# Kernel tuning notes

Hardware: AMD Instinct MI355X
Metric: run time of the kernel (lower is better)

## Reference

```python
import jax, jax.numpy as jnp
import numpy as np

B, T, D = 8, 4096, 1024
N_EXPERTS, N_SLOTS = 64, 8
HID = 256


def setup_inputs() -> dict:
    key = jax.random.key(0)
    ks = jax.random.split(key, 8)
    s = lambda *sh: 1.0 / np.sqrt(sh[-2]) if len(sh) >= 2 else 0.02
    tokens = jax.random.normal(ks[0], (B, T, D), dtype=jnp.float32)
    # routing weights, original uses np.random.random -> uniform [0,1); scale down for stability
    expert_mixture = jax.random.uniform(ks[1], (D, N_EXPERTS * N_SLOTS), dtype=jnp.float32) * 0.02
    W1 = jax.random.normal(ks[2], (N_EXPERTS, D, HID), dtype=jnp.float32) / np.sqrt(D)
    b1 = jnp.zeros((N_EXPERTS, HID), dtype=jnp.float32)
    W2 = jax.random.normal(ks[3], (N_EXPERTS, HID, HID), dtype=jnp.float32) / np.sqrt(HID)
    b2 = jnp.zeros((N_EXPERTS, HID), dtype=jnp.float32)
    W3 = jax.random.normal(ks[4], (N_EXPERTS, HID, D), dtype=jnp.float32) / np.sqrt(HID)
    b3 = jnp.zeros((N_EXPERTS, D), dtype=jnp.float32)
    return {"tokens": tokens, "expert_mixture": expert_mixture,
            "W1": W1, "b1": b1, "W2": W2, "b2": b2, "W3": W3, "b3": b3}


def reference(tokens, expert_mixture, W1, b1, W2, b2, W3, b3):
    b, t, d = tokens.shape
    flat = tokens.reshape(-1, d)                       # [BT, D]
    mat = flat @ expert_mixture                        # [BT, n*p]
    row_probs = jax.nn.softmax(mat, axis=0)            # over tokens
    col_probs = jax.nn.softmax(mat, axis=1)            # over slots
    x_hat = row_probs.T @ flat                         # [n*p, D] dispatch
    xs = x_hat.reshape(N_EXPERTS, N_SLOTS, d)          # [n, p, D]
    # per-expert MLP: Linear-ReLU-Linear-ReLU-Linear (batched over experts)
    h = jax.nn.relu(jnp.einsum('npd,ndh->nph', xs, W1) + b1[:, None, :])
    h = jax.nn.relu(jnp.einsum('nph,nhk->npk', h, W2) + b2[:, None, :])
    y_hat = jnp.einsum('npk,nkd->npd', h, W3) + b3[:, None, :]
    y_hat = y_hat.reshape(N_EXPERTS * N_SLOTS, d)      # [n*p, D]
    y = col_probs @ y_hat                              # [BT, D] combine
    return y.reshape(b, t, d)
```

## Files before the change

kernel.cpp:

```cpp
#include <hip/hip_runtime.h>
#include <math.h>

namespace {

constexpr int BT  = 8 * 4096;
constexpr int DIM = 1024;
constexpr int NE  = 64;
constexpr int NS  = 8;
constexpr int NP  = NE * NS;
constexpr int HID = 256;

typedef float f32x4 __attribute__((ext_vector_type(4)));
typedef __bf16 bf16x8 __attribute__((ext_vector_type(8)));
typedef short s16x8 __attribute__((ext_vector_type(8)));

__device__ __forceinline__ ushort f2bf(float x) {
  union { float f; unsigned u; } a; a.f = x;
  unsigned r = a.u + 0x7FFFu + ((a.u >> 16) & 1u);
  return (ushort)(r >> 16);
}
__device__ __forceinline__ float bf2f(ushort u) {
  union { unsigned u; float f; } a; a.u = (unsigned)u << 16;
  return a.f;
}

__device__ __forceinline__ void gload16(const void* g, void* l) {
  __builtin_amdgcn_global_load_lds(
      (const __attribute__((address_space(1))) void*)g,
      (__attribute__((address_space(3))) void*)l, 16, 0, 0);
}

template <bool ATOMIC, bool OBF, bool CSTAT>
__global__ __launch_bounds__(512) void k_gemm(const ushort* __restrict__ A,
                                              const ushort* __restrict__ Bt,
                                              void* __restrict__ Cv,
                                              int N, int kchunk,
                                              int lda, int ldb,
                                              float* __restrict__ pmOut,
                                              float* __restrict__ pzOut,
                                              float* __restrict__ rpmOut,
                                              float* __restrict__ rpzOut) {
  __shared__ __align__(16) ushort As0[256 * 64];
  __shared__ __align__(16) ushort As1[256 * 64];
  __shared__ __align__(16) ushort As2[256 * 64];
  __shared__ __align__(16) ushort Bs0[128 * 64];
  __shared__ __align__(16) ushort Bs1[128 * 64];
  __shared__ __align__(16) ushort Bs2[128 * 64];

  const int tid = threadIdx.x;
  const int wid = tid >> 6;
  const int lane = tid & 63;

  const int gx = gridDim.x, gy = gridDim.y;
  int wg = (blockIdx.z * gy + blockIdx.y) * gx + blockIdx.x;
  const int nwg = gx * gy * gridDim.z;
  wg = (wg & 7) * (nwg >> 3) + (wg >> 3);
  const int bx = wg % gx;
  const int rest = wg / gx;
  const int by = rest % gy;
  const int bz = rest / gy;

  const int n0 = bx * 128;
  const int m0 = by * 256;
  const int kb = bz * kchunk;

  const int w8 = wid * 8;
  const int lr = lane >> 3;
  const int ks = (((lane & 7) ^ lr) * 8);
  const ushort* Asrc = A + (size_t)(m0 + w8 + lr) * lda + ks;
  const ushort* Bsrc = Bt + (size_t)(n0 + w8 + lr) * ldb + ks;

  const int wm64 = (wid >> 1) * 64;
  const int wn64 = (wid & 1) * 64;
  const int fr = lane & 15;
  const int fq = lane >> 4;
  const int fq8 = fq * 8;
  const int frsw = (fr & 7) << 3;

  f32x4 acc[4][4];
#pragma unroll
  for (int i = 0; i < 4; ++i)
#pragma unroll
    for (int j = 0; j < 4; ++j) acc[i][j] = (f32x4){0.f, 0.f, 0.f, 0.f};

  const int nt = kchunk / 64;

#define STAGE6(An_, Bn_, kt_)                                                    \
  do {                                                                           \
    _Pragma("unroll") for (int q = 0; q < 4; ++q)                                \
      gload16(Asrc + (size_t)(q * 64) * lda + (kt_), (An_) + (q * 64 + w8) * 64);\
    _Pragma("unroll") for (int q = 0; q < 2; ++q)                                \
      gload16(Bsrc + (size_t)(q * 64) * ldb + (kt_), (Bn_) + (q * 64 + w8) * 64);\
  } while (0)

#define LD(B_, r_, h_)                                                          \
  __builtin_bit_cast(bf16x8, *(const s16x8*)((B_) + (size_t)(r_) * 64 +         \
                                             (((h_) * 32 + fq8) ^ frsw)))

#define GBLOCK(Ab_, Bb_, An_, Bn_, tt_)                                         \
  do {                                                                          \
    if ((tt_) + 1 < nt) asm volatile("s_waitcnt vmcnt(6)" ::: "memory");        \
    else                asm volatile("s_waitcnt vmcnt(0)" ::: "memory");        \
    __builtin_amdgcn_sched_barrier(0);                                          \
    __builtin_amdgcn_s_barrier();                                               \
    __builtin_amdgcn_sched_barrier(0);                                          \
    if ((tt_) + 2 < nt) STAGE6(An_, Bn_, kb + ((tt_) + 2) * 64);                \
    bf16x8 bfr_[4][2];                                                          \
    _Pragma("unroll") for (int n = 0; n < 4; ++n) {                             \
      bfr_[n][0] = LD(Bb_, wn64 + n * 16 + fr, 0);                              \
      bfr_[n][1] = LD(Bb_, wn64 + n * 16 + fr, 1);                              \
    }                                                                           \
    _Pragma("unroll") for (int m = 0; m < 4; ++m) {                             \
      bf16x8 a0_ = LD(Ab_, wm64 + m * 16 + fr, 0);                              \
      bf16x8 a1_ = LD(Ab_, wm64 + m * 16 + fr, 1);                              \
      __builtin_amdgcn_s_setprio(1);                                            \
      _Pragma("unroll") for (int n = 0; n < 4; ++n)                             \
        acc[m][n] = __builtin_amdgcn_mfma_f32_16x16x32_bf16(a0_, bfr_[n][0],    \
                                                            acc[m][n], 0, 0, 0);\
      _Pragma("unroll") for (int n = 0; n < 4; ++n)                             \
        acc[m][n] = __builtin_amdgcn_mfma_f32_16x16x32_bf16(a1_, bfr_[n][1],    \
                                                            acc[m][n], 0, 0, 0);\
      __builtin_amdgcn_s_setprio(0);                                            \
    }                                                                           \
  } while (0)

  STAGE6(As0, Bs0, kb);
  STAGE6(As1, Bs1, kb + 64);
  int t = 0;
  for (; t + 3 <= nt; t += 3) {
    GBLOCK(As0, Bs0, As2, Bs2, t);
    GBLOCK(As1, Bs1, As0, Bs0, t + 1);
    GBLOCK(As2, Bs2, As1, Bs1, t + 2);
  }
  if (t < nt) { GBLOCK(As0, Bs0, As2, Bs2, t); ++t; }
  if (t < nt) { GBLOCK(As1, Bs1, As0, Bs0, t); ++t; }
#undef GBLOCK
#undef LD
#undef STAGE6

  if (OBF) {
    ushort* Cb = (ushort*)Cv + (size_t)(m0 + wm64 + fq * 4) * N + n0 + wn64 + fr;
#pragma unroll
    for (int m = 0; m < 4; ++m)
#pragma unroll
      for (int n = 0; n < 4; ++n)
#pragma unroll
        for (int r = 0; r < 4; ++r)
          Cb[(size_t)(m * 16 + r) * N + n * 16] = f2bf(acc[m][n][r]);
  } else {
    float* Cb = (float*)Cv + (size_t)(m0 + wm64 + fq * 4) * N + n0 + wn64 + fr;
#pragma unroll
    for (int m = 0; m < 4; ++m)
#pragma unroll
      for (int n = 0; n < 4; ++n)
#pragma unroll
        for (int r = 0; r < 4; ++r) {
          float* p = Cb + (size_t)(m * 16 + r) * N + n * 16;
          if (ATOMIC) atomicAdd(p, acc[m][n][r]);
          else *p = acc[m][n][r];
        }
  }

  if (CSTAT) {
    float cm_[4], cz_[4];
#pragma unroll
    for (int n = 0; n < 4; ++n) { cm_[n] = -INFINITY; cz_[n] = 0.f; }
#pragma unroll
    for (int m = 0; m < 4; ++m)
#pragma unroll
      for (int n = 0; n < 4; ++n)
#pragma unroll
        for (int r = 0; r < 4; ++r) {
          float v = acc[m][n][r];
          float mm = fmaxf(cm_[n], v);
          cz_[n] = cz_[n] * __expf(cm_[n] - mm) + __expf(v - mm);
          cm_[n] = mm;
        }
#pragma unroll
    for (int off = 16; off <= 32; off <<= 1)
#pragma unroll
      for (int n = 0; n < 4; ++n) {
        float m2 = __shfl_xor(cm_[n], off);
        float z2 = __shfl_xor(cz_[n], off);
        float mm = fmaxf(cm_[n], m2);
        cz_[n] = cz_[n] * __expf(cm_[n] - mm) + z2 * __expf(m2 - mm);
        cm_[n] = mm;
      }
    float rm_[16], rz_[16];
#pragma unroll
    for (int m = 0; m < 4; ++m)
#pragma unroll
      for (int r = 0; r < 4; ++r) {
        const int i = m * 4 + r;
        float mx = fmaxf(fmaxf(acc[m][0][r], acc[m][1][r]),
                         fmaxf(acc[m][2][r], acc[m][3][r]));
        rm_[i] = mx;
        rz_[i] = __expf(acc[m][0][r] - mx) + __expf(acc[m][1][r] - mx) +
                 __expf(acc[m][2][r] - mx) + __expf(acc[m][3][r] - mx);
      }
#pragma unroll
    for (int off = 1; off <= 8; off <<= 1)
#pragma unroll
      for (int i = 0; i < 16; ++i) {
        float m2 = __shfl_xor(rm_[i], off);
        float z2 = __shfl_xor(rz_[i], off);
        float mm = fmaxf(rm_[i], m2);
        rz_[i] = rz_[i] * __expf(rm_[i] - mm) + z2 * __expf(m2 - mm);
        rm_[i] = mm;
      }
    __syncthreads();
    float* smx = (float*)As0;
    float* smz = smx + 4 * 128;
    float* smr = (float*)Bs0;
    float* smz2 = smr + 512;
    const int mrow = wid >> 1;
    if (lane < 16) {
#pragma unroll
      for (int n = 0; n < 4; ++n) {
        smx[mrow * 128 + wn64 + n * 16 + lane] = cm_[n];
        smz[mrow * 128 + wn64 + n * 16 + lane] = cz_[n];
      }
    }
    if (fr == 0) {
#pragma unroll
      for (int m = 0; m < 4; ++m)
#pragma unroll
        for (int r = 0; r < 4; ++r) {
          const int row = wm64 + m * 16 + fq * 4 + r;
          smr[(wid & 1) * 256 + row] = rm_[m * 4 + r];
          smz2[(wid & 1) * 256 + row] = rz_[m * 4 + r];
        }
    }
    __syncthreads();
    if (tid < 128) {
      float m = smx[tid], z = smz[tid];
#pragma unroll
      for (int p = 1; p < 4; ++p) {
        float m2 = smx[p * 128 + tid], z2 = smz[p * 128 + tid];
        float mm = fmaxf(m, m2);
        z = z * __expf(m - mm) + z2 * __expf(m2 - mm);
        m = mm;
      }
      pmOut[(size_t)by * NP + n0 + tid] = m;
      pzOut[(size_t)by * NP + n0 + tid] = z;
    }
    if (tid < 256) {
      float m1 = smr[tid], z1 = smz2[tid];
      float m2 = smr[256 + tid], z2 = smz2[256 + tid];
      float mm = fmaxf(m1, m2);
      float zz = z1 * __expf(m1 - mm) + z2 * __expf(m2 - mm);
      rpmOut[(size_t)bx * BT + m0 + tid] = mm;
      rpzOut[(size_t)bx * BT + m0 + tid] = zz;
    }
  }
}

__global__ __launch_bounds__(256) void k_convert(const float* __restrict__ X,
                                                 ushort* __restrict__ Y,
                                                 size_t n) {
  size_t i = ((size_t)blockIdx.x * 256 + threadIdx.x) * 8;
  const size_t stride = (size_t)gridDim.x * 256 * 8;
  for (; i < n; i += stride) {
    float4 a = *(const float4*)(X + i);
    float4 b = *(const float4*)(X + i + 4);
    s16x8 o;
    o[0] = (short)f2bf(a.x); o[1] = (short)f2bf(a.y);
    o[2] = (short)f2bf(a.z); o[3] = (short)f2bf(a.w);
    o[4] = (short)f2bf(b.x); o[5] = (short)f2bf(b.y);
    o[6] = (short)f2bf(b.z); o[7] = (short)f2bf(b.w);
    *(s16x8*)(Y + i) = o;
  }
}

__global__ __launch_bounds__(256) void k_tpose(const ushort* __restrict__ X,
                                               ushort* __restrict__ Yt,
                                               int Cc, int ldt) {
  __shared__ __align__(16) ushort tT[64][256];
  const int tid = threadIdx.x;
  const int r0 = blockIdx.x * 256, c0 = blockIdx.y * 64;
#pragma unroll
  for (int i = 0; i < 8; ++i) {
    const int idx = i * 256 + tid;
    const int r = idx >> 3, c8 = (idx & 7) * 8;
    s16x8 v = *(const s16x8*)(X + (size_t)(r0 + r) * Cc + c0 + c8);
#pragma unroll
    for (int j = 0; j < 8; ++j)
      tT[c8 + j][r ^ (((c8 + j) & 7) << 3)] = (ushort)v[j];
  }
  __syncthreads();
#pragma unroll
  for (int i = 0; i < 8; ++i) {
    const int idx = i * 256 + tid;
    const int c = idx >> 5, r8 = (idx & 31) * 8;
    s16x8 o = *(const s16x8*)&tT[c][r8 ^ ((c & 7) << 3)];
    *(s16x8*)(Yt + (size_t)(c0 + c) * ldt + r0 + r8) = o;
  }
}

template <bool ROWM, bool TRANSP>
__global__ __launch_bounds__(256) void k_cvt(const float* __restrict__ X,
                                             ushort* __restrict__ Yrm,
                                             ushort* __restrict__ Yt,
                                             int Cc, int ldt) {
  __shared__ __align__(16) ushort tT[64][256];
  const int tid = threadIdx.x;
  const int r0 = blockIdx.x * 256, c0 = blockIdx.y * 64;
#pragma unroll
  for (int i = 0; i < 16; ++i) {
    const int idx = i * 256 + tid;
    const int r = idx >> 4, c4 = (idx & 15) * 4;
    float4 v = *(const float4*)(X + (size_t)(r0 + r) * Cc + c0 + c4);
    ushort u[4] = {f2bf(v.x), f2bf(v.y), f2bf(v.z), f2bf(v.w)};
    if (ROWM) {
      ushort4 o = make_ushort4(u[0], u[1], u[2], u[3]);
      *(ushort4*)(Yrm + (size_t)(r0 + r) * Cc + c0 + c4) = o;
    }
    if (TRANSP) {
#pragma unroll
      for (int j = 0; j < 4; ++j)
        tT[c4 + j][r ^ (((c4 + j) & 7) << 3)] = u[j];
    }
  }
  if (TRANSP) {
    __syncthreads();
#pragma unroll
    for (int i = 0; i < 8; ++i) {
      const int idx = i * 256 + tid;
      const int c = idx >> 5, r8 = (idx & 31) * 8;
      s16x8 o = *(const s16x8*)&tT[c][r8 ^ ((c & 7) << 3)];
      *(s16x8*)(Yt + (size_t)(c0 + c) * ldt + r0 + r8) = o;
    }
  }
}

__global__ __launch_bounds__(256) void k_finals(const float* __restrict__ pm,
                                                const float* __restrict__ pz,
                                                const float* __restrict__ rpm,
                                                const float* __restrict__ rpz,
                                                float* __restrict__ colM,
                                                float* __restrict__ colIZ,
                                                float* __restrict__ rowM,
                                                float* __restrict__ rowIZ) {
  if (blockIdx.x < NP / 64) {
    const int col = blockIdx.x * 64 + (threadIdx.x & 63);
    const int q = threadIdx.x >> 6;
    float m = -INFINITY, z = 0.f;
    for (int r = q; r < BT / 256; r += 4) {
      float m2 = pm[(size_t)r * NP + col], z2 = pz[(size_t)r * NP + col];
      float mm = fmaxf(m, m2);
      z = z * __expf(m - mm) + z2 * __expf(m2 - mm);
      m = mm;
    }
    __shared__ float sm[4][64], sz[4][64];
    sm[q][threadIdx.x & 63] = m;
    sz[q][threadIdx.x & 63] = z;
    __syncthreads();
    if (q == 0) {
      for (int p = 1; p < 4; ++p) {
        float m2 = sm[p][threadIdx.x], z2 = sz[p][threadIdx.x];
        float mm = fmaxf(m, m2);
        z = z * __expf(m - mm) + z2 * __expf(m2 - mm);
        m = mm;
      }
      colM[col] = m;
      colIZ[col] = 1.f / z;
    }
  } else {
    const int t = (blockIdx.x - NP / 64) * 256 + threadIdx.x;
    float m = -INFINITY, z = 0.f;
#pragma unroll
    for (int c = 0; c < 4; ++c) {
      float m2 = rpm[(size_t)c * BT + t], z2 = rpz[(size_t)c * BT + t];
      float mm = fmaxf(m, m2);
      z = z * __expf(m - mm) + z2 * __expf(m2 - mm);
      m = mm;
    }
    rowM[t] = m;
    rowIZ[t] = 1.f / z;
  }
}

__global__ __launch_bounds__(256) void k_probs(const ushort* __restrict__ mat,
                                               const float* __restrict__ colM,
                                               const float* __restrict__ colIZ,
                                               const float* __restrict__ rowM,
                                               const float* __restrict__ rowIZ,
                                               ushort* __restrict__ Pc,
                                               ushort* __restrict__ Pt) {
  __shared__ __align__(16) ushort tT[64][256];
  __shared__ float cm[64], cz[64], rm[256], rz[256];
  const int tid = threadIdx.x;
  const int t0 = blockIdx.x * 256, s0 = blockIdx.y * 64;
  if (tid < 64) {
    cm[tid] = colM[s0 + tid];
    cz[tid] = colIZ[s0 + tid];
  }
  rm[tid] = rowM[t0 + tid];
  rz[tid] = rowIZ[t0 + tid];
  __syncthreads();
#pragma unroll
  for (int i = 0; i < 8; ++i) {
    const int idx = i * 256 + tid;
    const int r = idx >> 3, c8 = (idx & 7) * 8;
    s16x8 v = *(const s16x8*)(mat + (size_t)(t0 + r) * NP + s0 + c8);
    const float mr = rm[r], zr = rz[r];
    s16x8 oc;
#pragma unroll
    for (int j = 0; j < 8; ++j) {
      float f = bf2f((ushort)v[j]);
      oc[j] = (short)f2bf(__expf(f - mr) * zr);
      tT[c8 + j][r ^ (((c8 + j) & 7) << 3)] = f2bf(__expf(f - cm[c8 + j]) * cz[c8 + j]);
    }
    *(s16x8*)(Pc + (size_t)(t0 + r) * NP + s0 + c8) = oc;
  }
  __syncthreads();
#pragma unroll
  for (int i = 0; i < 8; ++i) {
    const int idx = i * 256 + tid;
    const int c = idx >> 5, r8 = (idx & 31) * 8;
    s16x8 o = *(const s16x8*)&tT[c][r8 ^ ((c & 7) << 3)];
    *(s16x8*)(Pt + (size_t)(s0 + c) * BT + t0 + r8) = o;
  }
}

__global__ __launch_bounds__(256) void k_binit3(const float* __restrict__ b1,
                                                const float* __restrict__ b2,
                                                const float* __restrict__ b3,
                                                float* __restrict__ base) {
  constexpr size_t XH = (size_t)NP * DIM;
  constexpr size_t H1 = (size_t)NP * HID;
  size_t idx = (size_t)blockIdx.x * 256 + threadIdx.x;
  if (idx < XH) { base[idx] = 0.f; return; }
  idx -= XH;
  if (idx < H1) { base[XH + idx] = b1[(idx / HID) / NS * HID + idx % HID]; return; }
  idx -= H1;
  if (idx < H1) { base[XH + H1 + idx] = b2[(idx / HID) / NS * HID + idx % HID]; return; }
  idx -= H1;
  base[XH + 2 * H1 + idx] = b3[(idx / DIM) / NS * DIM + idx % DIM];
}

template <int K, int N, int KS, bool RELU_IN>
__global__ __launch_bounds__(256) void k_mlp(const float* __restrict__ X,
                                             const float* __restrict__ W,
                                             float* __restrict__ Y) {
  constexpr int KSL = K / KS;
  __shared__ float xs[NS * KSL];
  const int tid = threadIdx.x;
  const int e = blockIdx.x;
  const int k0 = blockIdx.z * KSL;
  constexpr int T4 = (NS * KSL) / 4;
  for (int i = tid; i < T4; i += 256) {
    const int p = i / (KSL / 4), kk4 = (i % (KSL / 4)) * 4;
    float4 v = *(const float4*)(X + (size_t)(e * NS + p) * K + k0 + kk4);
    if (RELU_IN) {
      v.x = fmaxf(v.x, 0.f); v.y = fmaxf(v.y, 0.f);
      v.z = fmaxf(v.z, 0.f); v.w = fmaxf(v.w, 0.f);
    }
    *(float4*)(xs + p * KSL + kk4) = v;
  }
  __syncthreads();
  const int j = blockIdx.y * 64 + (tid & 63);
  const int pr = tid >> 6;
  const float* w = W + (size_t)e * K * N + (size_t)k0 * N + j;
  const float* x0 = xs + pr * KSL;
  const float* x1 = xs + (pr + 4) * KSL;
  float a0 = 0.f, a1 = 0.f;
#pragma unroll 8
  for (int k = 0; k < KSL; ++k) {
    float wv = w[(size_t)k * N];
    a0 += x0[k] * wv;
    a1 += x1[k] * wv;
  }
  atomicAdd(Y + (size_t)(e * NS + pr) * N + j, a0);
  atomicAdd(Y + (size_t)(e * NS + pr + 4) * N + j, a1);
}

}

extern "C" void kernel_launch(void* const* d_in, const int* in_sizes, int n_in,
                              void* d_out, int out_size, void* d_ws, size_t ws_size,
                              hipStream_t stream) {
  const float* tokens = (const float*)d_in[0];
  const float* em     = (const float*)d_in[1];
  const float* W1     = (const float*)d_in[2];
  const float* b1     = (const float*)d_in[3];
  const float* W2     = (const float*)d_in[4];
  const float* b2     = (const float*)d_in[5];
  const float* W3     = (const float*)d_in[6];
  const float* b3     = (const float*)d_in[7];
  float* out = (float*)d_out;

  char* w = (char*)d_ws;
  ushort* matb      = (ushort*)w; w += (size_t)BT * NP * 2;
  ushort* tokens_bf = (ushort*)w; w += (size_t)BT * DIM * 2;
  ushort* tokT      = (ushort*)w; w += (size_t)DIM * BT * 2;
  ushort* Pt        = (ushort*)w; w += (size_t)NP * BT * 2;
  ushort* Pc        = (ushort*)w; w += (size_t)BT * NP * 2;
  ushort* emT       = (ushort*)w; w += (size_t)NP * DIM * 2;
  ushort* yhatT     = (ushort*)w; w += (size_t)DIM * NP * 2;
  float*  pm        = (float*)w;  w += (size_t)(BT / 256) * NP * 4;
  float*  pz        = (float*)w;  w += (size_t)(BT / 256) * NP * 4;
  float*  rpm       = (float*)w;  w += (size_t)4 * BT * 4;
  float*  rpz       = (float*)w;  w += (size_t)4 * BT * 4;
  float*  colM      = (float*)w;  w += NP * 4;
  float*  colIZ     = (float*)w;  w += NP * 4;
  float*  rowM      = (float*)w;  w += BT * 4;
  float*  rowIZ     = (float*)w;  w += BT * 4;
  float*  xhat      = (float*)w;  w += (size_t)NP * DIM * 4;
  float*  h1        = (float*)w;  w += (size_t)NP * HID * 4;
  float*  h2        = (float*)w;  w += (size_t)NP * HID * 4;
  float*  yhat      = (float*)w;  w += (size_t)NP * DIM * 4;
  (void)ws_size; (void)in_sizes; (void)n_in; (void)out_size;

  k_convert<<<2048, 256, 0, stream>>>(tokens, tokens_bf, (size_t)BT * DIM);
  k_tpose<<<dim3(BT / 256, DIM / 64), 256, 0, stream>>>(tokens_bf, tokT, DIM, BT);
  k_cvt<false, true><<<dim3(DIM / 256, NP / 64), 256, 0, stream>>>(em, nullptr, emT, NP, DIM);
  k_gemm<false, true, true><<<dim3(NP / 128, BT / 256, 1), 512, 0, stream>>>(
      tokens_bf, emT, matb, NP, DIM, DIM, DIM, pm, pz, rpm, rpz);
  k_finals<<<NP / 64 + BT / 256, 256, 0, stream>>>(pm, pz, rpm, rpz, colM, colIZ, rowM, rowIZ);
  k_probs<<<dim3(BT / 256, NP / 64), 256, 0, stream>>>(matb, colM, colIZ, rowM, rowIZ, Pc, Pt);
  {
    constexpr size_t TOT = 2 * (size_t)NP * DIM + 2 * (size_t)NP * HID;
    k_binit3<<<(int)(TOT / 256), 256, 0, stream>>>(b1, b2, b3, xhat);
  }
  k_gemm<true, false, false><<<dim3(DIM / 128, NP / 256, 16), 512, 0, stream>>>(
      Pt, tokT, xhat, DIM, BT / 16, BT, BT, nullptr, nullptr, nullptr, nullptr);
  k_mlp<DIM, HID, 8, false><<<dim3(NE, HID / 64, 8), 256, 0, stream>>>(xhat, W1, h1);
  k_mlp<HID, HID, 4, true><<<dim3(NE, HID / 64, 4), 256, 0, stream>>>(h1, W2, h2);
  k_mlp<HID, DIM, 4, true><<<dim3(NE, DIM / 64, 4), 256, 0, stream>>>(h2, W3, yhat);
  k_cvt<false, true><<<dim3(NP / 256, DIM / 64), 256, 0, stream>>>(yhat, nullptr, yhatT, DIM, NP);
  k_gemm<false, false, false><<<dim3(DIM / 128, BT / 256, 1), 512, 0, stream>>>(
      Pc, yhatT, out, DIM, NP, NP, NP, nullptr, nullptr, nullptr, nullptr);
}
```

Before: 333.3 us.

## Fuse prep kernels and fold softmax finalization into split probability kernels

```diff
diff --git a/kernel.cpp b/kernel.cpp
--- a/kernel.cpp
+++ b/kernel.cpp
@@ -255,20 +255,74 @@
   }
 }
 
-__global__ __launch_bounds__(256) void k_convert(const float* __restrict__ X,
-                                                 ushort* __restrict__ Y,
-                                                 size_t n) {
-  size_t i = ((size_t)blockIdx.x * 256 + threadIdx.x) * 8;
-  const size_t stride = (size_t)gridDim.x * 256 * 8;
-  for (; i < n; i += stride) {
-    float4 a = *(const float4*)(X + i);
-    float4 b = *(const float4*)(X + i + 4);
-    s16x8 o;
-    o[0] = (short)f2bf(a.x); o[1] = (short)f2bf(a.y);
-    o[2] = (short)f2bf(a.z); o[3] = (short)f2bf(a.w);
-    o[4] = (short)f2bf(b.x); o[5] = (short)f2bf(b.y);
-    o[6] = (short)f2bf(b.z); o[7] = (short)f2bf(b.w);
-    *(s16x8*)(Y + i) = o;
+__global__ __launch_bounds__(256) void k_prep(const float* __restrict__ tokens,
+                                              const float* __restrict__ em,
+                                              const float* __restrict__ b1,
+                                              const float* __restrict__ b2,
+                                              const float* __restrict__ b3,
+                                              ushort* __restrict__ tokens_bf,
+                                              ushort* __restrict__ emT,
+                                              float* __restrict__ base) {
+  __shared__ __align__(16) ushort tT[64][256];
+  const int tid = threadIdx.x;
+  const int bid = blockIdx.x;
+  if (bid < 2048) {
+    const size_t n = (size_t)BT * DIM;
+    size_t i = ((size_t)bid * 256 + tid) * 8;
+    const size_t stride = (size_t)2048 * 256 * 8;
+    for (; i < n; i += stride) {
+      float4 a = *(const float4*)(tokens + i);
+      float4 b = *(const float4*)(tokens + i + 4);
+      s16x8 o;
+      o[0] = (short)f2bf(a.x); o[1] = (short)f2bf(a.y);
+      o[2] = (short)f2bf(a.z); o[3] = (short)f2bf(a.w);
+      o[4] = (short)f2bf(b.x); o[5] = (short)f2bf(b.y);
+      o[6] = (short)f2bf(b.z); o[7] = (short)f2bf(b.w);
+      *(s16x8*)(tokens_bf + i) = o;
+    }
+  } else if (bid < 2080) {
+    const int b = bid - 2048;
+    const int r0 = (b >> 3) * 256, c0 = (b & 7) * 64;
+#pragma unroll
+    for (int i = 0; i < 16; ++i) {
+      const int idx = i * 256 + tid;
+      const int r = idx >> 4, c4 = (idx & 15) * 4;
+      float4 v = *(const float4*)(em + (size_t)(r0 + r) * NP + c0 + c4);
+      ushort u[4] = {f2bf(v.x), f2bf(v.y), f2bf(v.z), f2bf(v.w)};
+#pragma unroll
+      for (int j = 0; j < 4; ++j)
+        tT[c4 + j][r ^ (((c4 + j) & 7) << 3)] = u[j];
+    }
+    __syncthreads();
+#pragma unroll
+    for (int i = 0; i < 8; ++i) {
+      const int idx = i * 256 + tid;
+      const int c = idx >> 5, r8 = (idx & 31) * 8;
+      s16x8 o = *(const s16x8*)&tT[c][r8 ^ ((c & 7) << 3)];
+      *(s16x8*)(emT + (size_t)(c0 + c) * DIM + r0 + r8) = o;
+    }
+  } else {
+    constexpr size_t XH = (size_t)NP * DIM;
+    constexpr size_t H1 = (size_t)NP * HID;
+    constexpr size_t TOT4 = (2 * XH + 2 * H1) / 4;
+    size_t i = (size_t)(bid - 2080) * 256 + tid;
+    for (; i < TOT4; i += (size_t)1024 * 256) {
+      const size_t idx = i * 4;
+      float4 v;
+      if (idx < XH) {
+        v = make_float4(0.f, 0.f, 0.f, 0.f);
+      } else if (idx < XH + H1) {
+        const size_t k = idx - XH;
+        v = *(const float4*)(b1 + (k / HID) / NS * HID + k % HID);
+      } else if (idx < XH + 2 * H1) {
+        const size_t k = idx - XH - H1;
+        v = *(const float4*)(b2 + (k / HID) / NS * HID + k % HID);
+      } else {
+        const size_t k = idx - XH - 2 * H1;
+        v = *(const float4*)(b3 + (k / DIM) / NS * DIM + k % DIM);
+      }
+      *(float4*)(base + idx) = v;
+    }
   }
 }
 
@@ -297,11 +351,9 @@
   }
 }
 
-template <bool ROWM, bool TRANSP>
-__global__ __launch_bounds__(256) void k_cvt(const float* __restrict__ X,
-                                             ushort* __restrict__ Yrm,
-                                             ushort* __restrict__ Yt,
-                                             int Cc, int ldt) {
+__global__ __launch_bounds__(256) void k_cvtT(const float* __restrict__ X,
+                                              ushort* __restrict__ Yt,
+                                              int Cc, int ldt) {
   __shared__ __align__(16) ushort tT[64][256];
   const int tid = threadIdx.x;
   const int r0 = blockIdx.x * 256, c0 = blockIdx.y * 64;
@@ -311,39 +363,67 @@
     const int r = idx >> 4, c4 = (idx & 15) * 4;
     float4 v = *(const float4*)(X + (size_t)(r0 + r) * Cc + c0 + c4);
     ushort u[4] = {f2bf(v.x), f2bf(v.y), f2bf(v.z), f2bf(v.w)};
-    if (ROWM) {
-      ushort4 o = make_ushort4(u[0], u[1], u[2], u[3]);
-      *(ushort4*)(Yrm + (size_t)(r0 + r) * Cc + c0 + c4) = o;
-    }
-    if (TRANSP) {
-#pragma unroll
-      for (int j = 0; j < 4; ++j)
-        tT[c4 + j][r ^ (((c4 + j) & 7) << 3)] = u[j];
-    }
-  }
-  if (TRANSP) {
-    __syncthreads();
-#pragma unroll
-    for (int i = 0; i < 8; ++i) {
-      const int idx = i * 256 + tid;
-      const int c = idx >> 5, r8 = (idx & 31) * 8;
-      s16x8 o = *(const s16x8*)&tT[c][r8 ^ ((c & 7) << 3)];
-      *(s16x8*)(Yt + (size_t)(c0 + c) * ldt + r0 + r8) = o;
-    }
-  }
-}
-
-__global__ __launch_bounds__(256) void k_finals(const float* __restrict__ pm,
-                                                const float* __restrict__ pz,
-                                                const float* __restrict__ rpm,
-                                                const float* __restrict__ rpz,
-                                                float* __restrict__ colM,
-                                                float* __restrict__ colIZ,
-                                                float* __restrict__ rowM,
-                                                float* __restrict__ rowIZ) {
-  if (blockIdx.x < NP / 64) {
-    const int col = blockIdx.x * 64 + (threadIdx.x & 63);
-    const int q = threadIdx.x >> 6;
+#pragma unroll
+    for (int j = 0; j < 4; ++j)
+      tT[c4 + j][r ^ (((c4 + j) & 7) << 3)] = u[j];
+  }
+  __syncthreads();
+#pragma unroll
+  for (int i = 0; i < 8; ++i) {
+    const int idx = i * 256 + tid;
+    const int c = idx >> 5, r8 = (idx & 31) * 8;
+    s16x8 o = *(const s16x8*)&tT[c][r8 ^ ((c & 7) << 3)];
+    *(s16x8*)(Yt + (size_t)(c0 + c) * ldt + r0 + r8) = o;
+  }
+}
+
+__global__ __launch_bounds__(256) void k_probs_c(const ushort* __restrict__ mat,
+                                                 const float* __restrict__ rpm,
+                                                 const float* __restrict__ rpz,
+                                                 ushort* __restrict__ Pc) {
+  __shared__ float rm[64], rz[64];
+  const int tid = threadIdx.x;
+  const int t0 = blockIdx.x * 64;
+  if (tid < 64) {
+    const int t = t0 + tid;
+    float m = -INFINITY, z = 0.f;
+#pragma unroll
+    for (int c = 0; c < 4; ++c) {
+      float m2 = rpm[(size_t)c * BT + t], z2 = rpz[(size_t)c * BT + t];
+      float mm = fmaxf(m, m2);
+      z = z * __expf(m - mm) + z2 * __expf(m2 - mm);
+      m = mm;
+    }
+    rm[tid] = m;
+    rz[tid] = 1.f / z;
+  }
+  __syncthreads();
+#pragma unroll
+  for (int i = 0; i < 16; ++i) {
+    const int idx = i * 256 + tid;
+    const int r = idx >> 6, c8 = (idx & 63) * 8;
+    s16x8 v = *(const s16x8*)(mat + (size_t)(t0 + r) * NP + c8);
+    const float mr = rm[r], zr = rz[r];
+    s16x8 oc;
+#pragma unroll
+    for (int j = 0; j < 8; ++j)
+      oc[j] = (short)f2bf(__expf(bf2f((ushort)v[j]) - mr) * zr);
+    *(s16x8*)(Pc + (size_t)(t0 + r) * NP + c8) = oc;
+  }
+}
+
+__global__ __launch_bounds__(256) void k_probs_t(const ushort* __restrict__ mat,
+                                                 const float* __restrict__ pm,
+                                                 const float* __restrict__ pz,
+                                                 ushort* __restrict__ Pt) {
+  __shared__ __align__(16) ushort tT[64][256];
+  __shared__ float cm[64], cz[64];
+  __shared__ float sm[4][64], sz[4][64];
+  const int tid = threadIdx.x;
+  const int t0 = blockIdx.x * 256, s0 = blockIdx.y * 64;
+  {
+    const int col = s0 + (tid & 63);
+    const int q = tid >> 6;
     float m = -INFINITY, z = 0.f;
     for (int r = q; r < BT / 256; r += 4) {
       float m2 = pm[(size_t)r * NP + col], z2 = pz[(size_t)r * NP + col];
@@ -351,67 +431,32 @@
       z = z * __expf(m - mm) + z2 * __expf(m2 - mm);
       m = mm;
     }
-    __shared__ float sm[4][64], sz[4][64];
-    sm[q][threadIdx.x & 63] = m;
-    sz[q][threadIdx.x & 63] = z;
-    __syncthreads();
-    if (q == 0) {
-      for (int p = 1; p < 4; ++p) {
-        float m2 = sm[p][threadIdx.x], z2 = sz[p][threadIdx.x];
-        float mm = fmaxf(m, m2);
-        z = z * __expf(m - mm) + z2 * __expf(m2 - mm);
-        m = mm;
-      }
-      colM[col] = m;
-      colIZ[col] = 1.f / z;
-    }
-  } else {
-    const int t = (blockIdx.x - NP / 64) * 256 + threadIdx.x;
-    float m = -INFINITY, z = 0.f;
-#pragma unroll
-    for (int c = 0; c < 4; ++c) {
-      float m2 = rpm[(size_t)c * BT + t], z2 = rpz[(size_t)c * BT + t];
+    sm[q][tid & 63] = m;
+    sz[q][tid & 63] = z;
+  }
+  __syncthreads();
+  if (tid < 64) {
+    float m = sm[0][tid], z = sz[0][tid];
+#pragma unroll
+    for (int p = 1; p < 4; ++p) {
+      float m2 = sm[p][tid], z2 = sz[p][tid];
       float mm = fmaxf(m, m2);
       z = z * __expf(m - mm) + z2 * __expf(m2 - mm);
       m = mm;
     }
-    rowM[t] = m;
-    rowIZ[t] = 1.f / z;
-  }
-}
-
-__global__ __launch_bounds__(256) void k_probs(const ushort* __restrict__ mat,
-                                               const float* __restrict__ colM,
-                                               const float* __restrict__ colIZ,
-                                               const float* __restrict__ rowM,
-                                               const float* __restrict__ rowIZ,
-                                               ushort* __restrict__ Pc,
-                                               ushort* __restrict__ Pt) {
-  __shared__ __align__(16) ushort tT[64][256];
-  __shared__ float cm[64], cz[64], rm[256], rz[256];
-  const int tid = threadIdx.x;
-  const int t0 = blockIdx.x * 256, s0 = blockIdx.y * 64;
-  if (tid < 64) {
-    cm[tid] = colM[s0 + tid];
-    cz[tid] = colIZ[s0 + tid];
-  }
-  rm[tid] = rowM[t0 + tid];
-  rz[tid] = rowIZ[t0 + tid];
+    cm[tid] = m;
+    cz[tid] = 1.f / z;
+  }
   __syncthreads();
 #pragma unroll
   for (int i = 0; i < 8; ++i) {
     const int idx = i * 256 + tid;
     const int r = idx >> 3, c8 = (idx & 7) * 8;
     s16x8 v = *(const s16x8*)(mat + (size_t)(t0 + r) * NP + s0 + c8);
-    const float mr = rm[r], zr = rz[r];
-    s16x8 oc;
-#pragma unroll
-    for (int j = 0; j < 8; ++j) {
-      float f = bf2f((ushort)v[j]);
-      oc[j] = (short)f2bf(__expf(f - mr) * zr);
-      tT[c8 + j][r ^ (((c8 + j) & 7) << 3)] = f2bf(__expf(f - cm[c8 + j]) * cz[c8 + j]);
-    }
-    *(s16x8*)(Pc + (size_t)(t0 + r) * NP + s0 + c8) = oc;
+#pragma unroll
+    for (int j = 0; j < 8; ++j)
+      tT[c8 + j][r ^ (((c8 + j) & 7) << 3)] =
+          f2bf(__expf(bf2f((ushort)v[j]) - cm[c8 + j]) * cz[c8 + j]);
   }
   __syncthreads();
 #pragma unroll
@@ -421,22 +466,6 @@
     s16x8 o = *(const s16x8*)&tT[c][r8 ^ ((c & 7) << 3)];
     *(s16x8*)(Pt + (size_t)(s0 + c) * BT + t0 + r8) = o;
   }
-}
-
-__global__ __launch_bounds__(256) void k_binit3(const float* __restrict__ b1,
-                                                const float* __restrict__ b2,
-                                                const float* __restrict__ b3,
-                                                float* __restrict__ base) {
-  constexpr size_t XH = (size_t)NP * DIM;
-  constexpr size_t H1 = (size_t)NP * HID;
-  size_t idx = (size_t)blockIdx.x * 256 + threadIdx.x;
-  if (idx < XH) { base[idx] = 0.f; return; }
-  idx -= XH;
-  if (idx < H1) { base[XH + idx] = b1[(idx / HID) / NS * HID + idx % HID]; return; }
-  idx -= H1;
-  if (idx < H1) { base[XH + H1 + idx] = b2[(idx / HID) / NS * HID + idx % HID]; return; }
-  idx -= H1;
-  base[XH + 2 * H1 + idx] = b3[(idx / DIM) / NS * DIM + idx % DIM];
 }
 
 template <int K, int N, int KS, bool RELU_IN>
@@ -502,33 +531,24 @@
   float*  pz        = (float*)w;  w += (size_t)(BT / 256) * NP * 4;
   float*  rpm       = (float*)w;  w += (size_t)4 * BT * 4;
   float*  rpz       = (float*)w;  w += (size_t)4 * BT * 4;
-  float*  colM      = (float*)w;  w += NP * 4;
-  float*  colIZ     = (float*)w;  w += NP * 4;
-  float*  rowM      = (float*)w;  w += BT * 4;
-  float*  rowIZ     = (float*)w;  w += BT * 4;
   float*  xhat      = (float*)w;  w += (size_t)NP * DIM * 4;
   float*  h1        = (float*)w;  w += (size_t)NP * HID * 4;
   float*  h2        = (float*)w;  w += (size_t)NP * HID * 4;
   float*  yhat      = (float*)w;  w += (size_t)NP * DIM * 4;
   (void)ws_size; (void)in_sizes; (void)n_in; (void)out_size;
 
-  k_convert<<<2048, 256, 0, stream>>>(tokens, tokens_bf, (size_t)BT * DIM);
+  k_prep<<<3104, 256, 0, stream>>>(tokens, em, b1, b2, b3, tokens_bf, emT, xhat);
   k_tpose<<<dim3(BT / 256, DIM / 64), 256, 0, stream>>>(tokens_bf, tokT, DIM, BT);
-  k_cvt<false, true><<<dim3(DIM / 256, NP / 64), 256, 0, stream>>>(em, nullptr, emT, NP, DIM);
   k_gemm<false, true, true><<<dim3(NP / 128, BT / 256, 1), 512, 0, stream>>>(
       tokens_bf, emT, matb, NP, DIM, DIM, DIM, pm, pz, rpm, rpz);
-  k_finals<<<NP / 64 + BT / 256, 256, 0, stream>>>(pm, pz, rpm, rpz, colM, colIZ, rowM, rowIZ);
-  k_probs<<<dim3(BT / 256, NP / 64), 256, 0, stream>>>(matb, colM, colIZ, rowM, rowIZ, Pc, Pt);
-  {
-    constexpr size_t TOT = 2 * (size_t)NP * DIM + 2 * (size_t)NP * HID;
-    k_binit3<<<(int)(TOT / 256), 256, 0, stream>>>(b1, b2, b3, xhat);
-  }
+  k_probs_c<<<BT / 64, 256, 0, stream>>>(matb, rpm, rpz, Pc);
+  k_probs_t<<<dim3(BT / 256, NP / 64), 256, 0, stream>>>(matb, pm, pz, Pt);
   k_gemm<true, false, false><<<dim3(DIM / 128, NP / 256, 16), 512, 0, stream>>>(
       Pt, tokT, xhat, DIM, BT / 16, BT, BT, nullptr, nullptr, nullptr, nullptr);
   k_mlp<DIM, HID, 8, false><<<dim3(NE, HID / 64, 8), 256, 0, stream>>>(xhat, W1, h1);
   k_mlp<HID, HID, 4, true><<<dim3(NE, HID / 64, 4), 256, 0, stream>>>(h1, W2, h2);
   k_mlp<HID, DIM, 4, true><<<dim3(NE, DIM / 64, 4), 256, 0, stream>>>(h2, W3, yhat);
-  k_cvt<false, true><<<dim3(NP / 256, DIM / 64), 256, 0, stream>>>(yhat, nullptr, yhatT, DIM, NP);
+  k_cvtT<<<dim3(NP / 256, DIM / 64), 256, 0, stream>>>(yhat, yhatT, DIM, NP);
   k_gemm<false, false, false><<<dim3(DIM / 128, BT / 256, 1), 512, 0, stream>>>(
       Pc, yhatT, out, DIM, NP, NP, NP, nullptr, nullptr, nullptr, nullptr);
 }
```

Measured after the change: 331.1 us. No clear change (-0.6%).
